# Kernel optimization log

Hardware: AMD Instinct MI355X
Metric: run time of the kernel (lower is better)

The kernel has to match this reference:

```python
import jax, jax.numpy as jnp
import numpy as np

NUM_HEADS, KEY_DIM, BLOCK, HALO = 8, 64, 8, 4
KV_KERNEL = BLOCK + 2 * HALO  # 16
EMB = NUM_HEADS * KEY_DIM     # 512


def setup_inputs() -> dict:
    key = jax.random.key(0)
    k = jax.random.split(key, 6)
    stddev = KEY_DIM ** -0.5
    return {
        "x": jax.random.normal(k[0], (8, 64, 64, 512), jnp.float32),
        "wq": jax.random.normal(k[1], (512, EMB), jnp.float32) * 0.02,
        "wkv": jax.random.normal(k[2], (512, 2 * EMB), jnp.float32) * 0.02,
        "wout": jax.random.normal(k[3], (EMB, EMB), jnp.float32) * 0.02,
        "pos_w": jax.random.normal(k[4], (KEY_DIM, 2 * KV_KERNEL - 1), jnp.float32) * stddev,
        "pos_h": jax.random.normal(k[5], (KEY_DIM, 2 * KV_KERNEL - 1), jnp.float32) * stddev,
    }


def rel_to_abs(rel):
    # rel: [B, N, hh, ww, 2*pos_dim-1] -> [B, N, hh, ww, pos_dim]
    b, n, hh, ww, dim = rel.shape
    pos_dim = (dim + 1) // 2
    gap = pos_dim - ww
    flat = rel.reshape(b, n, hh, ww * dim)[:, :, :, ww - 1:-1]
    return flat.reshape(b, n, hh, ww, 2 * (pos_dim - 1))[:, :, :, :, gap:pos_dim + gap]


def halo_forward(x, wq, wkv, wout, pos_w, pos_h):
    B, H, W, C = x.shape
    h, w = H // BLOCK, W // BLOCK
    K = KV_KERNEL
    scale = 1.0 / jnp.sqrt(jnp.asarray(KEY_DIM, x.dtype))

    # Query: [B, hd, h, w, block^2, key_dim]
    q = (x @ wq) * scale
    q = q.reshape(B, h, BLOCK, w, BLOCK, NUM_HEADS, KEY_DIM)
    attn_q = q.transpose(0, 5, 1, 3, 2, 4, 6).reshape(B, NUM_HEADS, h, w, BLOCK * BLOCK, KEY_DIM)

    # Overlapping halo KV windows (im2col-style gather, like tf.image.extract_patches)
    kv = x @ wkv
    kv_p = jnp.pad(kv, ((0, 0), (HALO, HALO), (HALO, HALO), (0, 0)))
    idx_h = jnp.arange(h)[:, None] * BLOCK + jnp.arange(K)[None, :]  # [h, K]
    idx_w = jnp.arange(w)[:, None] * BLOCK + jnp.arange(K)[None, :]  # [w, K]
    patches = kv_p[:, idx_h][:, :, :, idx_w]          # [B, h, K, w, K, 2*EMB]
    patches = patches.transpose(0, 1, 3, 2, 4, 5)     # [B, h, w, K, K, 2*EMB]
    patches = patches.reshape(B, h, w, K * K, NUM_HEADS, 2 * KEY_DIM)
    patches = patches.transpose(0, 4, 1, 2, 3, 5)     # [B, hd, h, w, K^2, 2*key_dim]
    key_t, val = patches[..., :KEY_DIM], patches[..., KEY_DIM:]

    scores = jnp.einsum('bnhwqc,bnhwkc->bnhwqk', attn_q, key_t)  # [B,hd,h,w,bq,bk]

    # Relative position logits (width + height), query already carries qk_scale
    pos_q = attn_q.reshape(B, NUM_HEADS * h * w, BLOCK, BLOCK, KEY_DIM)
    rel_w = rel_to_abs(pos_q @ pos_w)                                      # [B,N,hb,wb,K]
    rel_h = rel_to_abs(pos_q.transpose(0, 1, 3, 2, 4) @ pos_h)
    rel_h = rel_h.transpose(0, 1, 3, 2, 4)                                 # [B,N,hb,wb,K]
    pos = rel_w[..., None, :] + rel_h[..., :, None]                        # [B,N,hb,wb,Kh,Kw]
    pos = pos.reshape(B, NUM_HEADS, h, w, BLOCK * BLOCK, K * K)

    attn = jax.nn.softmax(scores + pos, axis=-1)
    out = jnp.einsum('bnhwqk,bnhwkc->bnhwqc', attn, val)
    out = out.reshape(B, NUM_HEADS, h, w, BLOCK, BLOCK, KEY_DIM)
    out = out.transpose(0, 2, 4, 3, 5, 1, 6).reshape(B, H, W, EMB)
    return out @ wout


def reference(x, wq, wkv, wout, pos_w, pos_h):
    return halo_forward(x, wq, wkv, wout, pos_w, pos_h)
```

## Files before the change

### kernel.cpp

```cpp
#include <hip/hip_runtime.h>
#include <hip/hip_fp16.h>
#include <math.h>

typedef _Float16 f16x8 __attribute__((ext_vector_type(8)));
typedef _Float16 f16x4 __attribute__((ext_vector_type(4)));
typedef float    f32x4 __attribute__((ext_vector_type(4)));

#define M_TOT 32768
#define VROW  4608
#define LOG2E 1.44269504088896f

__device__ __forceinline__ void gload16(const void* g, void* l) {
    __builtin_amdgcn_global_load_lds(
        (const __attribute__((address_space(1))) unsigned int*)g,
        (__attribute__((address_space(3))) unsigned int*)l, 16, 0, 0);
}

__device__ __forceinline__ f32x4 mfma32(f16x8 a, f16x8 b, f32x4 c) {
    return __builtin_amdgcn_mfma_f32_16x16x32_f16(a, b, c, 0, 0, 0);
}

__global__ __launch_bounds__(256) void prep(
    const float* __restrict__ x, const float* __restrict__ wq,
    const float* __restrict__ wkv, const float* __restrict__ wout,
    const float* __restrict__ posw, const float* __restrict__ posh,
    __half* __restrict__ x16, __half* __restrict__ wT, __half* __restrict__ woT,
    __half* __restrict__ posT, __half* __restrict__ vTp, __half* __restrict__ zp)
{
    const int bid = blockIdx.x, t = threadIdx.x;
    if (bid < 8192) {
        const size_t i = ((size_t)bid * 256 + t) * 8;
        float4 a = *(const float4*)&x[i];
        float4 b = *(const float4*)&x[i + 4];
        __half2 h[4];
        h[0] = __floats2half2_rn(a.x, a.y);
        h[1] = __floats2half2_rn(a.z, a.w);
        h[2] = __floats2half2_rn(b.x, b.y);
        h[3] = __floats2half2_rn(b.z, b.w);
        *(float4*)&x16[i] = *(float4*)h;
    } else if (bid < 12288) {
        const int id = (bid - 8192) * 256 + t;
        const int nr = id >> 9, k = id & 511;
        if (nr < 512) {
            wT[(size_t)nr * 512 + k] = __float2half(wq[k * 512 + nr] * (0.125f * LOG2E));
        } else if (nr < 1536) {
            wT[(size_t)nr * 512 + k] = __float2half(wkv[k * 1024 + (nr - 512)]);
        } else {
            woT[(size_t)(nr - 1536) * 512 + k] = __float2half(wout[k * 512 + (nr - 1536)]);
        }
    } else if (bid < 14336) {
        const int id = (bid - 12288) * 256 + t;
        const int row = id >> 7, rem = id & 127;
        const int y = rem >> 1, side = rem & 1;
        f16x4 z = {(_Float16)0.f, (_Float16)0.f, (_Float16)0.f, (_Float16)0.f};
        *(f16x4*)(vTp + (size_t)row * VROW + y * 72 + side * 68) = z;
    } else if (bid < 14352) {
        const int id = (bid - 14336) * 256 + t;
        const int tb = id >> 11, idx = (id >> 6) & 31, d = id & 63;
        const float* src = tb ? posh : posw;
        posT[id] = __float2half((idx < 31) ? src[d * 31 + idx] : 0.f);
    } else {
        if (t < 16) {
            float4 z = make_float4(0.f, 0.f, 0.f, 0.f);
            *(float4*)(zp + t * 8) = z;
        }
    }
}

template <int MODE, int NBN>
__global__ __launch_bounds__(256) void mfma_gemm(
    const __half* __restrict__ A, const __half* __restrict__ Bt,
    __half* __restrict__ q16, __half* __restrict__ k16, __half* __restrict__ vTp,
    float* __restrict__ outf)
{
    __shared__ __align__(16) char As[2 * 16384];
    __shared__ __align__(16) char Bs[2 * 16384];

    const int t = threadIdx.x;
    const int l = t & 63, w = t >> 6;
    const int wr = w >> 1, wc = w & 1;
    const int lr = l & 15, hi = l >> 4;

    const int bid = blockIdx.x;
    const int xcd = bid & 7, loc = bid >> 3;
    const int half = loc / (16 * NBN);
    const int rem  = loc % (16 * NBN);
    const int bn   = rem >> 4;
    const int bm   = xcd * 32 + half * 16 + (rem & 15);

    f32x4 acc[4][4];
    #pragma unroll
    for (int i = 0; i < 4; ++i)
        #pragma unroll
        for (int j = 0; j < 4; ++j) acc[i][j] = (f32x4){0.f, 0.f, 0.f, 0.f};

    const int sch = (t & 7);
    const int srw = (t >> 3);

    auto STAGE = [&](int sel, int k0) {
        #pragma unroll
        for (int it = 0; it < 4; ++it) {
            const int row = it * 32 + srw;
            const int kk  = k0 + ((sch ^ (row & 7)) * 8);
            gload16(A + (size_t)(bm * 128 + row) * 512 + kk,
                    As + sel * 16384 + (it * 256 + w * 64) * 16);
        }
        #pragma unroll
        for (int it = 0; it < 4; ++it) {
            const int row = it * 32 + srw;
            const int kk  = k0 + ((sch ^ (row & 7)) * 8);
            gload16(Bt + (size_t)(bn * 128 + row) * 512 + kk,
                    Bs + sel * 16384 + (it * 256 + w * 64) * 16);
        }
    };

    STAGE(0, 0);
    asm volatile("s_waitcnt vmcnt(0)" ::: "memory");
    __builtin_amdgcn_s_barrier();

    #pragma unroll
    for (int k0 = 0; k0 < 512; k0 += 64) {
        const int sel = (k0 >> 6) & 1;
        if (k0 < 448) STAGE(sel ^ 1, k0 + 64);

        const char* Ab = As + sel * 16384;
        const char* Bb = Bs + sel * 16384;
        #pragma unroll
        for (int dc = 0; dc < 2; ++dc) {
            f16x8 af[4], bf[4];
            #pragma unroll
            for (int i = 0; i < 4; ++i) {
                const int ra = wr * 64 + i * 16 + lr;
                af[i] = *(const f16x8*)(Ab + ra * 128 + (((dc * 4 + hi) ^ (ra & 7)) * 16));
            }
            #pragma unroll
            for (int j = 0; j < 4; ++j) {
                const int rb = wc * 64 + j * 16 + lr;
                bf[j] = *(const f16x8*)(Bb + rb * 128 + (((dc * 4 + hi) ^ (rb & 7)) * 16));
            }
            #pragma unroll
            for (int i = 0; i < 4; ++i)
                #pragma unroll
                for (int j = 0; j < 4; ++j)
                    acc[i][j] = mfma32(af[i], bf[j], acc[i][j]);
        }

        if (k0 < 448) {
            asm volatile("s_waitcnt vmcnt(0)" ::: "memory");
            __builtin_amdgcn_s_barrier();
        }
    }

    const int lq = hi;
    #pragma unroll
    for (int i = 0; i < 4; ++i) {
        #pragma unroll
        for (int j = 0; j < 4; ++j) {
            const int row0 = bm * 128 + wr * 64 + i * 16 + lq * 4;
            const int col  = bn * 128 + wc * 64 + j * 16 + lr;
            if (MODE == 1) {
                #pragma unroll
                for (int r = 0; r < 4; ++r)
                    outf[(size_t)(row0 + r) * 512 + col] = acc[i][j][r];
            } else if (bn < 4) {
                #pragma unroll
                for (int r = 0; r < 4; ++r)
                    q16[(size_t)(row0 + r) * 512 + col] = __float2half(acc[i][j][r]);
            } else if (wc == 0) {
                const int head = bn - 4, d2 = j * 16 + lr;
                #pragma unroll
                for (int r = 0; r < 4; ++r)
                    k16[(size_t)(row0 + r) * 512 + head * 64 + d2] = __float2half(acc[i][j][r]);
            } else {
                const int head = bn - 4, d2 = j * 16 + lr;
                const int bb = row0 >> 12, pix = row0 & 4095;
                const int py = pix >> 6, px = pix & 63;
                f16x4 pv;
                #pragma unroll
                for (int r = 0; r < 4; ++r) pv[r] = (_Float16)acc[i][j][r];
                *(f16x4*)(vTp + ((size_t)((bb * 8 + head) * 64 + d2)) * VROW + py * 72 + px + 4) = pv;
            }
        }
    }
}

__global__ __launch_bounds__(256, 4) void halo_attn(
    const __half* __restrict__ qbuf, const __half* __restrict__ kbuf,
    const __half* __restrict__ vTp, const __half* __restrict__ posT,
    const __half* __restrict__ zp, __half* __restrict__ obuf)
{
    __shared__ __align__(16) char KP[64 * 520];
    __shared__ __align__(16) char POSB[6336];
    __shared__ float red[4][64];

    __half* RW = (__half*)POSB;
    __half* RH = (__half*)(POSB + 3168);
    float (*red2)[64] = (float(*)[64])POSB;

    const int hw = blockIdx.x;
    const int wg = (hw & 7) * 512 + (hw >> 3);
    const int wb = wg & 7, hb = (wg >> 3) & 7, n = (wg >> 6) & 7, b = wg >> 9;
    const int t = threadIdx.x;
    const int l = t & 63, g = t >> 6;
    const int hi = l >> 4, c15 = l & 15;

    #pragma unroll
    for (int it = 0; it < 8; ++it) {
        const int cid = it * 256 + t;
        const int S = cid * 16;
        const int row = S >> 7;
        const int d0h = (((S & 127) >> 4) ^ (row & 7)) * 8;
        const int ky = hb * 8 - 4 + (row >> 4);
        const int kx = wb * 8 - 4 + (row & 15);
        const bool ok = ((unsigned)ky < 64u) && ((unsigned)kx < 64u);
        const __half* src = ok ? (kbuf + ((size_t)((b * 64 + ky) * 64 + kx)) * 512 + n * 64 + d0h)
                               : zp;
        gload16(src, KP + (it * 256 + g * 64) * 16);
    }

    f16x8 vfrag[8];
    {
        const __half* vrow = vTp + ((size_t)((b * 8 + n) * 64 + g * 16 + c15)) * VROW;
        const int xoff = wb * 8 + (hi & 1) * 8;
        #pragma unroll
        for (int kc = 0; kc < 8; ++kc) {
            const int ki = kc * 2 + (hi >> 1);
            const int y = hb * 8 - 4 + ki;
            const __half* p = ((unsigned)y < 64u) ? (vrow + y * 72 + xoff) : zp;
            vfrag[kc] = *(const f16x8*)p;
        }
    }

    f16x8 qreg[4][2];
    #pragma unroll
    for (int qf = 0; qf < 4; ++qf) {
        const int q = qf * 16 + c15;
        const size_t pix = (size_t)((b * 64 + hb * 8 + (q >> 3)) * 64 + wb * 8 + (q & 7));
        #pragma unroll
        for (int dc = 0; dc < 2; ++dc)
            qreg[qf][dc] = *(const f16x8*)(qbuf + pix * 512 + n * 64 + dc * 32 + hi * 8);
    }

    {
        const int tb = g >> 1, ih = g & 1;
        f32x4 accp[4];
        #pragma unroll
        for (int qf = 0; qf < 4; ++qf) accp[qf] = (f32x4){0.f, 0.f, 0.f, 0.f};
        #pragma unroll
        for (int dc = 0; dc < 2; ++dc) {
            const f16x8 a = *(const f16x8*)(posT + tb * 2048 + (ih * 16 + c15) * 64 + dc * 32 + hi * 8);
            #pragma unroll
            for (int qf = 0; qf < 4; ++qf)
                accp[qf] = mfma32(a, qreg[qf][dc], accp[qf]);
        }
        __half* dst = tb ? RH : RW;
        #pragma unroll
        for (int qf = 0; qf < 4; ++qf)
            #pragma unroll
            for (int r = 0; r < 4; ++r) {
                const unsigned idx8 = (unsigned)(ih * 16 + hi * 4 + r) - 8u;
                if (idx8 < 23u)
                    dst[idx8 * 66 + qf * 16 + c15] = __float2half(accp[qf][r]);
            }
    }
    __syncthreads();

    f32x4 accs[4][4];
    #pragma unroll
    for (int kf = 0; kf < 4; ++kf)
        #pragma unroll
        for (int qf = 0; qf < 4; ++qf) accs[kf][qf] = (f32x4){0.f, 0.f, 0.f, 0.f};

    __builtin_amdgcn_s_setprio(1);
    #pragma unroll
    for (int kf = 0; kf < 4; ++kf) {
        const int row = g * 64 + kf * 16 + c15;
        #pragma unroll
        for (int dc = 0; dc < 2; ++dc) {
            const int off = (row * 128 + dc * 64 + hi * 16) ^ ((row & 7) << 4);
            f16x8 a = *(const f16x8*)(KP + off);
            #pragma unroll
            for (int qf = 0; qf < 4; ++qf)
                accs[kf][qf] = mfma32(a, qreg[qf][dc], accs[kf][qf]);
        }
    }
    __builtin_amdgcn_s_setprio(0);

    float mq[4];
    #pragma unroll
    for (int qf = 0; qf < 4; ++qf) {
        const int q = qf * 16 + c15;
        const int qj = q & 7, qi = q >> 3;
        float pa[4], pb[4];
        #pragma unroll
        for (int r = 0; r < 4; ++r)  pa[r] = __half2float(RW[(hi * 4 + r + 7 - qj) * 66 + q]);
        #pragma unroll
        for (int kf = 0; kf < 4; ++kf) pb[kf] = __half2float(RH[(g * 4 + kf + 7 - qi) * 66 + q]);
        float mm = -1e30f;
        #pragma unroll
        for (int kf = 0; kf < 4; ++kf)
            #pragma unroll
            for (int r = 0; r < 4; ++r) {
                const float s = accs[kf][qf][r] + pa[r] + pb[kf];
                accs[kf][qf][r] = s;
                mm = fmaxf(mm, s);
            }
        mm = fmaxf(mm, __shfl_xor(mm, 16));
        mm = fmaxf(mm, __shfl_xor(mm, 32));
        mq[qf] = mm;
    }
    if (l < 16) {
        #pragma unroll
        for (int qf = 0; qf < 4; ++qf) red[g][qf * 16 + l] = mq[qf];
    }
    __syncthreads();

    float sums[4];
    #pragma unroll
    for (int qf = 0; qf < 4; ++qf) {
        const int q = qf * 16 + c15;
        const float mfull = fmaxf(fmaxf(red[0][q], red[1][q]), fmaxf(red[2][q], red[3][q]));
        float ss = 0.f;
        #pragma unroll
        for (int kf = 0; kf < 4; ++kf)
            #pragma unroll
            for (int r = 0; r < 4; ++r) {
                const float p = exp2f(accs[kf][qf][r] - mfull);
                accs[kf][qf][r] = p;
                ss += p;
            }
        ss += __shfl_xor(ss, 16);
        ss += __shfl_xor(ss, 32);
        sums[qf] = ss;
        #pragma unroll
        for (int kf = 0; kf < 4; ++kf) {
            __half2 h01 = __floats2half2_rn(accs[kf][qf][0], accs[kf][qf][1]);
            __half2 h23 = __floats2half2_rn(accs[kf][qf][2], accs[kf][qf][3]);
            uint2 wv;
            wv.x = *(unsigned*)&h01;
            wv.y = *(unsigned*)&h23;
            *(uint2*)(KP + q * 520 + (g * 64 + kf * 16 + hi * 4) * 2) = wv;
        }
    }
    if (l < 16) {
        #pragma unroll
        for (int qf = 0; qf < 4; ++qf) red2[g][qf * 16 + l] = sums[qf];
    }
    __syncthreads();

    f32x4 acco[4];
    #pragma unroll
    for (int qf = 0; qf < 4; ++qf) acco[qf] = (f32x4){0.f, 0.f, 0.f, 0.f};
    __builtin_amdgcn_s_setprio(1);
    #pragma unroll
    for (int kc = 0; kc < 8; ++kc) {
        const f16x8 bf = vfrag[kc];
        #pragma unroll
        for (int qf = 0; qf < 4; ++qf) {
            const char* pp = KP + (qf * 16 + c15) * 520 + kc * 64 + hi * 16;
            const f16x4 p0 = *(const f16x4*)pp;
            const f16x4 p1 = *(const f16x4*)(pp + 8);
            const f16x8 af = __builtin_shufflevector(p0, p1, 0, 1, 2, 3, 4, 5, 6, 7);
            acco[qf] = mfma32(af, bf, acco[qf]);
        }
    }
    __builtin_amdgcn_s_setprio(0);

    #pragma unroll
    for (int qf = 0; qf < 4; ++qf) {
        #pragma unroll
        for (int r = 0; r < 4; ++r) {
            const int q = qf * 16 + hi * 4 + r;
            const float den = red2[0][q] + red2[1][q] + red2[2][q] + red2[3][q];
            const float v = acco[qf][r] * __builtin_amdgcn_rcpf(den);
            const size_t pix = (size_t)((b * 64 + hb * 8 + (q >> 3)) * 64 + wb * 8 + (q & 7));
            obuf[pix * 512 + n * 64 + g * 16 + c15] = __float2half(v);
        }
    }
}

extern "C" void kernel_launch(void* const* d_in, const int* in_sizes, int n_in,
                              void* d_out, int out_size, void* d_ws, size_t ws_size,
                              hipStream_t stream)
{
    const float* x    = (const float*)d_in[0];
    const float* wq   = (const float*)d_in[1];
    const float* wkv  = (const float*)d_in[2];
    const float* wout = (const float*)d_in[3];
    const float* posw = (const float*)d_in[4];
    const float* posh = (const float*)d_in[5];
    float* out = (float*)d_out;

    const size_t NPIX = (size_t)M_TOT * 512;
    const size_t NVTP = (size_t)64 * 64 * VROW;
    __half* x16  = (__half*)d_ws;
    __half* wT   = x16 + NPIX;
    __half* woT  = wT + (size_t)1536 * 512;
    __half* q16  = woT + (size_t)512 * 512;
    __half* k16  = q16 + NPIX;
    __half* vTp  = k16 + NPIX;
    __half* o16  = vTp + NVTP;
    __half* zp   = o16 + NPIX;
    __half* posT = zp + 128;

    prep<<<14353, 256, 0, stream>>>(x, wq, wkv, wout, posw, posh,
                                    x16, wT, woT, posT, vTp, zp);

    mfma_gemm<0, 12><<<3072, 256, 0, stream>>>(x16, wT, q16, k16, vTp, nullptr);

    halo_attn<<<4096, 256, 0, stream>>>(q16, k16, vTp, posT, zp, o16);

    mfma_gemm<1, 4><<<1024, 256, 0, stream>>>(o16, woT, nullptr, nullptr, nullptr, out);
}
```

Before: 204.1 us.

## Use triple-buffered K=32 stages with partial vmcnt waits in MFMA GEMM

Restructures the GEMM main loop from double-buffered K=64 tiles into a three-stage ring of K=32 tiles. Each step waits only on the older outstanding loads (vmcnt(4)), so two loads stay in flight while compute runs, and only one barrier is taken per step. The LDS layout changes to a chunk-major arrangement with no XOR swizzle, and shared memory per block shrinks, which could allow higher occupancy. The trade-off is twice as many barriers, and the unswizzled layout may cause LDS bank conflicts on the fragment reads.

```diff
diff --git a/kernel.cpp b/kernel.cpp
--- a/kernel.cpp
+++ b/kernel.cpp
@@ -73,8 +73,8 @@
     __half* __restrict__ q16, __half* __restrict__ k16, __half* __restrict__ vTp,
     float* __restrict__ outf)
 {
-    __shared__ __align__(16) char As[2 * 16384];
-    __shared__ __align__(16) char Bs[2 * 16384];
+    __shared__ __align__(16) char As[3 * 8192];
+    __shared__ __align__(16) char Bs[3 * 8192];
 
     const int t = threadIdx.x;
     const int l = t & 63, w = t >> 6;
@@ -94,61 +94,54 @@
         #pragma unroll
         for (int j = 0; j < 4; ++j) acc[i][j] = (f32x4){0.f, 0.f, 0.f, 0.f};
 
-    const int sch = (t & 7);
-    const int srw = (t >> 3);
+    const int srow = t & 127;
+    const int sc0  = t >> 7;
+    const size_t arow = (size_t)(bm * 128 + srow) * 512;
+    const size_t brow = (size_t)(bn * 128 + srow) * 512;
 
     auto STAGE = [&](int sel, int k0) {
         #pragma unroll
-        for (int it = 0; it < 4; ++it) {
-            const int row = it * 32 + srw;
-            const int kk  = k0 + ((sch ^ (row & 7)) * 8);
-            gload16(A + (size_t)(bm * 128 + row) * 512 + kk,
-                    As + sel * 16384 + (it * 256 + w * 64) * 16);
-        }
-        #pragma unroll
-        for (int it = 0; it < 4; ++it) {
-            const int row = it * 32 + srw;
-            const int kk  = k0 + ((sch ^ (row & 7)) * 8);
-            gload16(Bt + (size_t)(bn * 128 + row) * 512 + kk,
-                    Bs + sel * 16384 + (it * 256 + w * 64) * 16);
+        for (int it = 0; it < 2; ++it) {
+            const int chunk = it * 2 + sc0;
+            gload16(A + arow + k0 + chunk * 8,
+                    As + sel * 8192 + (it * 256 + w * 64) * 16);
+        }
+        #pragma unroll
+        for (int it = 0; it < 2; ++it) {
+            const int chunk = it * 2 + sc0;
+            gload16(Bt + brow + k0 + chunk * 8,
+                    Bs + sel * 8192 + (it * 256 + w * 64) * 16);
         }
     };
 
+    auto COMPUTE = [&](int sel) {
+        const char* Ab = As + sel * 8192;
+        const char* Bb = Bs + sel * 8192;
+        f16x8 af[4], bf[4];
+        #pragma unroll
+        for (int i = 0; i < 4; ++i)
+            af[i] = *(const f16x8*)(Ab + (hi * 128 + wr * 64 + i * 16 + lr) * 16);
+        #pragma unroll
+        for (int j = 0; j < 4; ++j)
+            bf[j] = *(const f16x8*)(Bb + (hi * 128 + wc * 64 + j * 16 + lr) * 16);
+        #pragma unroll
+        for (int i = 0; i < 4; ++i)
+            #pragma unroll
+            for (int j = 0; j < 4; ++j)
+                acc[i][j] = mfma32(af[i], bf[j], acc[i][j]);
+    };
+
     STAGE(0, 0);
-    asm volatile("s_waitcnt vmcnt(0)" ::: "memory");
-    __builtin_amdgcn_s_barrier();
-
-    #pragma unroll
-    for (int k0 = 0; k0 < 512; k0 += 64) {
-        const int sel = (k0 >> 6) & 1;
-        if (k0 < 448) STAGE(sel ^ 1, k0 + 64);
-
-        const char* Ab = As + sel * 16384;
-        const char* Bb = Bs + sel * 16384;
-        #pragma unroll
-        for (int dc = 0; dc < 2; ++dc) {
-            f16x8 af[4], bf[4];
-            #pragma unroll
-            for (int i = 0; i < 4; ++i) {
-                const int ra = wr * 64 + i * 16 + lr;
-                af[i] = *(const f16x8*)(Ab + ra * 128 + (((dc * 4 + hi) ^ (ra & 7)) * 16));
-            }
-            #pragma unroll
-            for (int j = 0; j < 4; ++j) {
-                const int rb = wc * 64 + j * 16 + lr;
-                bf[j] = *(const f16x8*)(Bb + rb * 128 + (((dc * 4 + hi) ^ (rb & 7)) * 16));
-            }
-            #pragma unroll
-            for (int i = 0; i < 4; ++i)
-                #pragma unroll
-                for (int j = 0; j < 4; ++j)
-                    acc[i][j] = mfma32(af[i], bf[j], acc[i][j]);
-        }
-
-        if (k0 < 448) {
-            asm volatile("s_waitcnt vmcnt(0)" ::: "memory");
-            __builtin_amdgcn_s_barrier();
-        }
+    STAGE(1, 32);
+
+    #pragma unroll
+    for (int k = 0; k < 16; ++k) {
+        if (k == 15) { asm volatile("s_waitcnt vmcnt(0)" ::: "memory"); }
+        else         { asm volatile("s_waitcnt vmcnt(4)" ::: "memory"); }
+        __builtin_amdgcn_s_barrier();
+        __builtin_amdgcn_sched_barrier(0);
+        if (k < 14) STAGE((k + 2) % 3, (k + 2) * 32);
+        COMPUTE(k % 3);
     }
 
     const int lq = hi;
```

Measured after the change: 249.7 us. 1.22x slower.
